# Optimization experiments

Measured on AMD Instinct MI355X. Metric: run time of the kernel, lower is better.

The kernel has to match this reference:

```python
import jax, jax.numpy as jnp
import numpy as np

EPS = 1e-12  # torch F.normalize eps

def _cam(fmap, w):
    # torch: sum over C of w[1,C,R,1,1] * fmap[B,C,1,H,W] -> (B,R,H,W)
    # expressed as an efficient contraction (1x1 conv / GEMM)
    return jnp.einsum('bchw,rc->brhw', fmap, w)

def _embedding(fmap, w, b):
    pooled = fmap.mean(axis=(-2, -1))           # (B,C) AdaptiveAvgPool2d(1)
    return pooled @ w.T + b                      # (B,R)

def _certainty(cam):
    B, R = cam.shape[:2]
    flat = cam.reshape(B, R, -1)
    return jnp.std(flat, axis=-1, ddof=1)        # torch .std() is unbiased

def _avgpool_to(x, out_hw):
    # adaptive avg pool with integer ratio == reshape-mean
    B, R, H, W = x.shape
    oh, ow = out_hw
    return x.reshape(B, R, oh, H // oh, ow, W // ow).mean(axis=(3, 5))

def _link(low_cam, high_cam):
    low_cam = jax.lax.stop_gradient(low_cam)
    high_cam = jax.lax.stop_gradient(high_cam)
    if low_cam.shape[2:] != high_cam.shape[2:]:
        low_cam = _avgpool_to(low_cam, high_cam.shape[2:])
    B = low_cam.shape[0]
    lo = low_cam.reshape(B, low_cam.shape[1], -1)
    hi = high_cam.reshape(B, high_cam.shape[1], -1)
    lo = lo / jnp.maximum(jnp.linalg.norm(lo, axis=-1, keepdims=True), EPS)
    hi = hi / jnp.maximum(jnp.linalg.norm(hi, axis=-1, keepdims=True), EPS)
    return jnp.einsum('bmi,bni->mn', lo, hi) / B

def setup_inputs() -> dict:
    key = jax.random.key(0)
    ks = jax.random.split(key, 6)
    B, R = 64, 128
    chans = [512, 1024, 2048]
    hws = [28, 14, 7]
    inp = {}
    for l in range(3):
        inp[f'fmap{l}'] = jax.random.normal(ks[l], (B, chans[l], hws[l], hws[l]), dtype=jnp.float32)
        inp[f'w{l}'] = jax.random.normal(ks[3 + l], (R, chans[l]), dtype=jnp.float32) * 0.02
        inp[f'b{l}'] = jnp.zeros((R,), dtype=jnp.float32)
    return inp

def reference(fmap0, fmap1, fmap2, w0, b0, w1, b1, w2, b2):
    fmaps = [fmap0, fmap1, fmap2]
    ws = [w0, w1, w2]
    bs = [b0, b1, b2]
    embeddings = [_embedding(f, w, b) for f, w, b in zip(fmaps, ws, bs)]
    cams = [_cam(f, w) for f, w in zip(fmaps, ws)]
    certainties = [_certainty(c) for c in cams]
    links = [_link(cams[l - 1], cams[l]) for l in range(1, 3)]
    return (*embeddings, *certainties, *links)
```

## Files before the change

kernel.cpp:

```cpp
#include <hip/hip_runtime.h>
#include <stdint.h>

#define R 128
#define NB 64

#define CAM0_OFF 0
#define CAM1_OFF 6422528
#define CAM2_OFF 8028160
#define POOL0_OFF 8429568
#define POOL1_OFF 10035200
#define WB_OFF    10436608
#define PART_OFF  10665984
#define NORM_OFF  12763136

typedef __bf16 bf16;
typedef bf16 v2bf __attribute__((ext_vector_type(2)));
typedef bf16 v8bf __attribute__((ext_vector_type(8)));
typedef float f4v __attribute__((ext_vector_type(4)));

#define ASM_BARRIER() asm volatile("s_waitcnt lgkmcnt(0)\n\ts_barrier" ::: "memory")

__global__ void prep_w(const float* __restrict__ w0, const float* __restrict__ w1,
                       const float* __restrict__ w2, bf16* __restrict__ wb) {
    int id = blockIdx.x * 256 + threadIdx.x;
    float v;
    if (id < 65536)       v = w0[id];
    else if (id < 196608) v = w1[id - 65536];
    else                  v = w2[id - 196608];
    wb[id] = (bf16)v;
}

__global__ __launch_bounds__(512) void cam_gemm(
    const float* __restrict__ f0, const float* __restrict__ f1,
    const float* __restrict__ f2, const bf16* __restrict__ wb,
    float* __restrict__ ws) {
    __shared__ bf16 ldsB[2][64 * 72];

    int bid = blockIdx.x, tid = threadIdx.x;
    int lvl, b, i0;
    if (bid < 64)       { lvl = 2; b = bid; i0 = 0; }
    else if (bid < 320) { int t = bid - 64; lvl = 1; b = t >> 2;
                          int ti = t & 3; i0 = ti < 3 ? ti * 64 : 132; }
    else                { int t = bid - 320; lvl = 0; b = t / 13;
                          int ti = t - b * 13; i0 = ti < 12 ? ti * 64 : 720; }
    const int C  = (lvl == 0) ? 512 : (lvl == 1) ? 1024 : 2048;
    const int HW = (lvl == 0) ? 784 : (lvl == 1) ? 196  : 49;
    const float* fmap = (lvl == 0) ? f0 : (lvl == 1) ? f1 : f2;
    const bf16*  wbl  = wb + ((lvl == 0) ? 0 : (lvl == 1) ? 65536 : 196608);
    float* cam = ws + ((lvl == 0) ? CAM0_OFF : (lvl == 1) ? CAM1_OFF : CAM2_OFF);

    int d = tid >> 4;
    int ku2 = d * 2;
    int i4 = (tid & 15) * 4;
    int gbase = b * C * HW + ku2 * HW + i0 + i4;
    int ldsd[4];
    int i4c[4];
#pragma unroll
    for (int e = 0; e < 4; ++e) {
        int i = i4 + e;
        int grp = (d >> 2) ^ ((i >> 3) & 7);
        ldsd[e] = i * 72 + grp * 8 + (d & 3) * 2;
        i4c[e] = min(i, 48);
    }
    const int lane = tid & 63, wave = tid >> 6;
    const int lm = lane & 15, q = lane >> 4;
    const int wm = (wave >> 1) * 32, wn = (wave & 1) * 32;
    int irow[2], ixor[2];
#pragma unroll
    for (int sn = 0; sn < 2; ++sn) {
        irow[sn] = wn + sn * 16 + lm;
        ixor[sn] = (irow[sn] >> 3) & 7;
    }
    const bf16* arow[2];
#pragma unroll
    for (int sm = 0; sm < 2; ++sm)
        arow[sm] = wbl + (wm + sm * 16 + lm) * C + q * 8;

    auto loadT = [&](int kc, float4 (&r)[2]) {
        if (HW != 49) {
            const float* p = fmap + gbase + kc * HW;
            r[0] = *(const float4*)p;
            r[1] = *(const float4*)(p + HW);
        } else {
            const float* p = fmap + b * C * 49 + (kc + ku2) * 49;
            r[0].x = p[i4c[0]]; r[0].y = p[i4c[1]];
            r[0].z = p[i4c[2]]; r[0].w = p[i4c[3]];
            r[1].x = p[49 + i4c[0]]; r[1].y = p[49 + i4c[1]];
            r[1].z = p[49 + i4c[2]]; r[1].w = p[49 + i4c[3]];
        }
    };
    auto stage = [&](float4 (&r)[2], bf16* buf) {
        v2bf t0 = { (bf16)r[0].x, (bf16)r[1].x };
        v2bf t1 = { (bf16)r[0].y, (bf16)r[1].y };
        v2bf t2 = { (bf16)r[0].z, (bf16)r[1].z };
        v2bf t3 = { (bf16)r[0].w, (bf16)r[1].w };
        *(v2bf*)&buf[ldsd[0]] = t0;
        *(v2bf*)&buf[ldsd[1]] = t1;
        *(v2bf*)&buf[ldsd[2]] = t2;
        *(v2bf*)&buf[ldsd[3]] = t3;
    };

    f4v acc[2][2] = {};
    auto comp = [&](int kc, const bf16* buf) {
#pragma unroll
        for (int ks = 0; ks < 64; ks += 32) {
            v8bf af[2];
#pragma unroll
            for (int sm = 0; sm < 2; ++sm)
                af[sm] = *(const v8bf*)(arow[sm] + kc + ks);
            v8bf bfr[2];
#pragma unroll
            for (int sn = 0; sn < 2; ++sn) {
                int grp = (q + ((ks >> 5) << 2)) ^ ixor[sn];
                bfr[sn] = *(const v8bf*)&buf[irow[sn] * 72 + grp * 8];
            }
#pragma unroll
            for (int sm = 0; sm < 2; ++sm)
#pragma unroll
                for (int sn = 0; sn < 2; ++sn)
                    acc[sm][sn] = __builtin_amdgcn_mfma_f32_16x16x32_bf16(
                        af[sm], bfr[sn], acc[sm][sn], 0, 0, 0);
        }
    };

    const int nIter = C >> 6;
    float4 rT[4][2];
    loadT(0, rT[0]); loadT(64, rT[1]); loadT(128, rT[2]); loadT(192, rT[3]);
    for (int t = 0; t < nIter; t += 4) {
#pragma unroll
        for (int u = 0; u < 4; ++u) {
            stage(rT[u], ldsB[u & 1]);
            ASM_BARRIER();
            if (t + u + 4 < nIter) loadT((t + u + 4) << 6, rT[u]);
            comp((t + u) << 6, ldsB[u & 1]);
        }
    }
#pragma unroll
    for (int sn = 0; sn < 2; ++sn) {
        int i_n = i0 + irow[sn];
        if (i_n < HW) {
            int base = (b * R) * HW + i_n;
#pragma unroll
            for (int sm = 0; sm < 2; ++sm) {
#pragma unroll
                for (int reg = 0; reg < 4; ++reg) {
                    int r = wm + sm * 16 + q * 4 + reg;
                    cam[base + r * HW] = acc[sm][sn][reg];
                }
            }
        }
    }
}

__global__ __launch_bounds__(256) void post_k(
    float* __restrict__ ws, const float* __restrict__ b0,
    const float* __restrict__ b1, const float* __restrict__ b2,
    float* __restrict__ out) {
    __shared__ float plds[4 * 784];
    int gw = blockIdx.x * 4 + (threadIdx.x >> 6);
    int lane = threadIdx.x & 63;
    float* myl = plds + (threadIdx.x >> 6) * 784;
    int lvl = gw >> 13, row = gw & 8191;
    const int HW = (lvl == 0) ? 784 : (lvl == 1) ? 196 : 49;
    const float* cam = ws + ((lvl == 0) ? CAM0_OFF : (lvl == 1) ? CAM1_OFF : CAM2_OFF)
                        + (long)row * HW;
    float s = 0.f, ss = 0.f;
    for (int j = lane; j < HW; j += 64) {
        float v = cam[j]; s += v; ss += v * v; myl[j] = v;
    }
#pragma unroll
    for (int o = 32; o; o >>= 1) { s += __shfl_xor(s, o); ss += __shfl_xor(ss, o); }
    if (lane == 0) {
        const float* bias = (lvl == 0) ? b0 : (lvl == 1) ? b1 : b2;
        float mean = s / (float)HW;
        out[lvl * 8192 + row] = mean + bias[row & 127];
        float var = fmaxf(ss - s * mean, 0.f) / (float)(HW - 1);
        out[24576 + lvl * 8192 + row] = sqrtf(var);
        if (lvl >= 1)
            ws[NORM_OFF + (lvl - 1) * 8192 + row] = 1.0f / fmaxf(sqrtf(ss), 1e-12f);
    }
    if (lvl <= 1) {
        const int OP = (lvl == 0) ? 196 : 49;
        const int OW = (lvl == 0) ? 14 : 7;
        const int IW = (lvl == 0) ? 28 : 14;
        float vals[4]; float ssp = 0.f; int cnt = 0;
        for (int p = lane; p < OP; p += 64) {
            int oh = p / OW, ow = p - oh * OW;
            int i0 = oh * 2 * IW + ow * 2;
            float v = (myl[i0] + myl[i0 + 1] + myl[i0 + IW] + myl[i0 + IW + 1]) * 0.25f;
            vals[cnt++] = v; ssp += v * v;
        }
#pragma unroll
        for (int o = 32; o; o >>= 1) ssp += __shfl_xor(ssp, o);
        float inv = 1.0f / fmaxf(sqrtf(ssp), 1e-12f);
        float* dst = ws + ((lvl == 0) ? POOL0_OFF : POOL1_OFF) + (long)row * OP;
        cnt = 0;
        for (int p = lane; p < OP; p += 64) dst[p] = vals[cnt++] * inv;
    }
}

__device__ inline v8bf load_frag8(const float* __restrict__ row, int k0, int K) {
    v8bf f;
    if (k0 + 8 <= K && (K & 3) == 0) {
        float4 a = *(const float4*)(row + k0);
        float4 c = *(const float4*)(row + k0 + 4);
        f[0] = (bf16)a.x; f[1] = (bf16)a.y; f[2] = (bf16)a.z; f[3] = (bf16)a.w;
        f[4] = (bf16)c.x; f[5] = (bf16)c.y; f[6] = (bf16)c.z; f[7] = (bf16)c.w;
    } else {
#pragma unroll
        for (int j = 0; j < 8; ++j)
            f[j] = (k0 + j < K) ? (bf16)row[k0 + j] : (bf16)0.f;
    }
    return f;
}

__global__ __launch_bounds__(256) void link_mfma_k(const float* __restrict__ ws,
                                                   float* __restrict__ part) {
    int bid = blockIdx.x, tid = threadIdx.x;
    int lk = bid >> 7, rem = bid & 127;
    int b = rem >> 1, mh = rem & 1;
    const int K = lk ? 49 : 196;
    const float* lo = ws + (lk ? POOL1_OFF : POOL0_OFF) + (long)(b * 128 + mh * 64) * K;
    const float* hi = ws + (lk ? CAM2_OFF : CAM1_OFF) + (long)b * 128 * K;
    const float* nrmp = ws + NORM_OFF + lk * 8192 + b * 128;
    int lane = tid & 63, wv = tid >> 6;
    int lm = lane & 15, q = lane >> 4;
    int wm = (wv >> 1) * 32, wn = (wv & 1) * 64;
    f4v acc[2][4] = {};
    for (int kc = 0; kc < K; kc += 32) {
        v8bf af[2], bff[4];
#pragma unroll
        for (int sm = 0; sm < 2; ++sm)
            af[sm] = load_frag8(lo + (long)(wm + sm * 16 + lm) * K, kc + q * 8, K);
#pragma unroll
        for (int sn = 0; sn < 4; ++sn)
            bff[sn] = load_frag8(hi + (long)(wn + sn * 16 + lm) * K, kc + q * 8, K);
#pragma unroll
        for (int sm = 0; sm < 2; ++sm)
#pragma unroll
            for (int sn = 0; sn < 4; ++sn)
                acc[sm][sn] = __builtin_amdgcn_mfma_f32_16x16x32_bf16(
                    af[sm], bff[sn], acc[sm][sn], 0, 0, 0);
    }
    float* pb = part + (long)b * 32768 + lk * 16384;
#pragma unroll
    for (int sn = 0; sn < 4; ++sn) {
        int n = wn + sn * 16 + lm;
        float sh = nrmp[n];
#pragma unroll
        for (int sm = 0; sm < 2; ++sm) {
#pragma unroll
            for (int reg = 0; reg < 4; ++reg) {
                int m = mh * 64 + wm + sm * 16 + q * 4 + reg;
                pb[m * 128 + n] = acc[sm][sn][reg] * sh;
            }
        }
    }
}

__global__ void linkred_k(const float* __restrict__ part, float* __restrict__ out) {
    int id = blockIdx.x * 256 + threadIdx.x;
    float s0 = 0.f, s1 = 0.f, s2 = 0.f, s3 = 0.f;
#pragma unroll
    for (int b = 0; b < 64; b += 4) {
        s0 += part[(long)(b + 0) * 32768 + id];
        s1 += part[(long)(b + 1) * 32768 + id];
        s2 += part[(long)(b + 2) * 32768 + id];
        s3 += part[(long)(b + 3) * 32768 + id];
    }
    out[49152 + id] = (s0 + s1 + s2 + s3) * (1.0f / 64.0f);
}

extern "C" void kernel_launch(void* const* d_in, const int* in_sizes, int n_in,
                              void* d_out, int out_size, void* d_ws, size_t ws_size,
                              hipStream_t stream) {
    const float* f0 = (const float*)d_in[0];
    const float* w0 = (const float*)d_in[1];
    const float* b0 = (const float*)d_in[2];
    const float* f1 = (const float*)d_in[3];
    const float* w1 = (const float*)d_in[4];
    const float* b1 = (const float*)d_in[5];
    const float* f2 = (const float*)d_in[6];
    const float* w2 = (const float*)d_in[7];
    const float* b2 = (const float*)d_in[8];
    float* ws = (float*)d_ws;
    float* out = (float*)d_out;
    bf16* wb = (bf16*)(ws + WB_OFF);

    prep_w<<<1792, 256, 0, stream>>>(w0, w1, w2, wb);
    cam_gemm<<<1152, 512, 0, stream>>>(f0, f1, f2, wb, ws);
    post_k<<<6144, 256, 0, stream>>>(ws, b0, b1, b2, out);
    link_mfma_k<<<256, 256, 0, stream>>>(ws, ws + PART_OFF);
    linkred_k<<<128, 256, 0, stream>>>(ws + PART_OFF, out);
}
```

Before: 296.6 us.

## Fuse CAM statistics and pooling into GEMM epilogue, atomically reduce link outputs

The GEMM now tiles spatial positions in 56-wide chunks aligned to image rows. Its epilogue computes per-row sums, sums of squares and 2x2 pooled values from an LDS tile, accumulating them with atomics. This stops the level-0 CAM from being written to global memory, and the separate post kernel becomes a small finalize kernel. The link kernel applies both normalisations and atomically adds into the output, which removes the partial buffer and its reduction kernel. The cost is atomic contention, extra work in the GEMM epilogue, and more GEMM blocks because of the 56-wide tiling.

```diff
diff --git a/kernel.cpp b/kernel.cpp
--- a/kernel.cpp
+++ b/kernel.cpp
@@ -4,14 +4,16 @@
 #define R 128
 #define NB 64
 
-#define CAM0_OFF 0
-#define CAM1_OFF 6422528
-#define CAM2_OFF 8028160
-#define POOL0_OFF 8429568
-#define POOL1_OFF 10035200
-#define WB_OFF    10436608
-#define PART_OFF  10665984
-#define NORM_OFF  12763136
+#define CAM1_OFF  0
+#define CAM2_OFF  1605632
+#define POOL0_OFF 2007040
+#define POOL1_OFF 3612672
+#define WB_OFF    4014080
+#define ACCS_OFF  4243456
+#define ACCQ_OFF  4268032
+#define PSQ_OFF   4292608
+#define INVHI_OFF 4308992
+#define INVLO_OFF 4325376
 
 typedef __bf16 bf16;
 typedef bf16 v2bf __attribute__((ext_vector_type(2)));
@@ -21,8 +23,11 @@
 #define ASM_BARRIER() asm volatile("s_waitcnt lgkmcnt(0)\n\ts_barrier" ::: "memory")
 
 __global__ void prep_w(const float* __restrict__ w0, const float* __restrict__ w1,
-                       const float* __restrict__ w2, bf16* __restrict__ wb) {
+                       const float* __restrict__ w2, bf16* __restrict__ wb,
+                       float* __restrict__ ws, float* __restrict__ out) {
     int id = blockIdx.x * 256 + threadIdx.x;
+    if (id < 65536) ws[ACCS_OFF + id] = 0.f;
+    if (id < 32768) out[49152 + id] = 0.f;
     float v;
     if (id < 65536)       v = w0[id];
     else if (id < 196608) v = w1[id - 65536];
@@ -34,25 +39,26 @@
     const float* __restrict__ f0, const float* __restrict__ f1,
     const float* __restrict__ f2, const bf16* __restrict__ wb,
     float* __restrict__ ws) {
-    __shared__ bf16 ldsB[2][64 * 72];
+    __shared__ __align__(16) char ldsRaw[34816];
+#define LBUF(u) ((bf16*)ldsRaw + (u) * (64 * 72))
 
     int bid = blockIdx.x, tid = threadIdx.x;
-    int lvl, b, i0;
-    if (bid < 64)       { lvl = 2; b = bid; i0 = 0; }
+    int lvl, b, i0, VW;
+    if (bid < 64)       { lvl = 2; b = bid; i0 = 0; VW = 49; }
     else if (bid < 320) { int t = bid - 64; lvl = 1; b = t >> 2;
-                          int ti = t & 3; i0 = ti < 3 ? ti * 64 : 132; }
-    else                { int t = bid - 320; lvl = 0; b = t / 13;
-                          int ti = t - b * 13; i0 = ti < 12 ? ti * 64 : 720; }
+                          int ti = t & 3; i0 = ti * 56; VW = ti < 3 ? 56 : 28; }
+    else                { int t = bid - 320; lvl = 0; b = t / 14;
+                          int ti = t - b * 14; i0 = ti * 56; VW = 56; }
     const int C  = (lvl == 0) ? 512 : (lvl == 1) ? 1024 : 2048;
     const int HW = (lvl == 0) ? 784 : (lvl == 1) ? 196  : 49;
     const float* fmap = (lvl == 0) ? f0 : (lvl == 1) ? f1 : f2;
     const bf16*  wbl  = wb + ((lvl == 0) ? 0 : (lvl == 1) ? 65536 : 196608);
-    float* cam = ws + ((lvl == 0) ? CAM0_OFF : (lvl == 1) ? CAM1_OFF : CAM2_OFF);
 
     int d = tid >> 4;
     int ku2 = d * 2;
     int i4 = (tid & 15) * 4;
-    int gbase = b * C * HW + ku2 * HW + i0 + i4;
+    int i4eff = min(i4, VW - 4);
+    int gbase = b * C * HW + ku2 * HW + i0 + i4eff;
     int ldsd[4];
     int i4c[4];
 #pragma unroll
@@ -77,7 +83,7 @@
         arow[sm] = wbl + (wm + sm * 16 + lm) * C + q * 8;
 
     auto loadT = [&](int kc, float4 (&r)[2]) {
-        if (HW != 49) {
+        if (lvl != 2) {
             const float* p = fmap + gbase + kc * HW;
             r[0] = *(const float4*)p;
             r[1] = *(const float4*)(p + HW);
@@ -129,74 +135,98 @@
     for (int t = 0; t < nIter; t += 4) {
 #pragma unroll
         for (int u = 0; u < 4; ++u) {
-            stage(rT[u], ldsB[u & 1]);
+            stage(rT[u], LBUF(u & 1));
             ASM_BARRIER();
             if (t + u + 4 < nIter) loadT((t + u + 4) << 6, rT[u]);
-            comp((t + u) << 6, ldsB[u & 1]);
-        }
-    }
-#pragma unroll
-    for (int sn = 0; sn < 2; ++sn) {
-        int i_n = i0 + irow[sn];
-        if (i_n < HW) {
-            int base = (b * R) * HW + i_n;
-#pragma unroll
-            for (int sm = 0; sm < 2; ++sm) {
-#pragma unroll
-                for (int reg = 0; reg < 4; ++reg) {
-                    int r = wm + sm * 16 + q * 4 + reg;
-                    cam[base + r * HW] = acc[sm][sn][reg];
-                }
+            comp((t + u) << 6, LBUF(u & 1));
+        }
+    }
+
+    __syncthreads();
+    float* tile = (float*)ldsRaw;
+#pragma unroll
+    for (int sn = 0; sn < 2; ++sn)
+#pragma unroll
+        for (int sm = 0; sm < 2; ++sm)
+#pragma unroll
+            for (int reg = 0; reg < 4; ++reg)
+                tile[(wm + sm * 16 + q * 4 + reg) * 68 + wn + sn * 16 + lm] =
+                    acc[sm][sn][reg];
+    __syncthreads();
+
+    int row = tid >> 2, seg = tid & 3;
+    long grow = (long)b * 128 + row;
+    const float* trow = tile + row * 68;
+    float* camrow = (lvl == 1) ? ws + CAM1_OFF + grow * 196 + i0
+                  : (lvl == 2) ? ws + CAM2_OFF + grow * 49 : (float*)0;
+    float s = 0.f, qq = 0.f;
+    const f4v* tr4 = (const f4v*)(trow + seg * 16);
+#pragma unroll
+    for (int g = 0; g < 4; ++g) {
+        f4v v4 = tr4[g];
+#pragma unroll
+        for (int e = 0; e < 4; ++e) {
+            int col = seg * 16 + g * 4 + e;
+            if (col < VW) {
+                float v = v4[e];
+                s += v; qq += v * v;
+                if (lvl) camrow[col] = v;
             }
         }
     }
-}
-
-__global__ __launch_bounds__(256) void post_k(
+    s += __shfl_xor(s, 1);  s += __shfl_xor(s, 2);
+    qq += __shfl_xor(qq, 1); qq += __shfl_xor(qq, 2);
+    if (seg == 0) {
+        atomicAdd(&ws[ACCS_OFF + lvl * 8192 + grow], s);
+        atomicAdd(&ws[ACCQ_OFF + lvl * 8192 + grow], qq);
+    }
+    if (lvl == 0) {
+        float ps = 0.f;
+        float* prow = ws + POOL0_OFF + grow * 196 + (i0 / 56) * 14;
+        for (int j = seg; j < 14; j += 4) {
+            float v = 0.25f * (trow[2 * j] + trow[2 * j + 1] +
+                               trow[28 + 2 * j] + trow[28 + 2 * j + 1]);
+            prow[j] = v; ps += v * v;
+        }
+        ps += __shfl_xor(ps, 1); ps += __shfl_xor(ps, 2);
+        if (seg == 0) atomicAdd(&ws[PSQ_OFF + grow], ps);
+    } else if (lvl == 1) {
+        float ps = 0.f;
+        int tt = i0 / 56;
+        int npj = (VW == 56) ? 14 : 7;
+        for (int pj = seg; pj < npj; pj += 4) {
+            int sub = pj / 7, jj = pj - sub * 7;
+            const float* tr2 = trow + sub * 28;
+            float v = 0.25f * (tr2[2 * jj] + tr2[2 * jj + 1] +
+                               tr2[14 + 2 * jj] + tr2[14 + 2 * jj + 1]);
+            ws[POOL1_OFF + grow * 49 + (2 * tt + sub) * 7 + jj] = v;
+            ps += v * v;
+        }
+        ps += __shfl_xor(ps, 1); ps += __shfl_xor(ps, 2);
+        if (seg == 0) atomicAdd(&ws[PSQ_OFF + 8192 + grow], ps);
+    }
+#undef LBUF
+}
+
+__global__ __launch_bounds__(256) void finalize_k(
     float* __restrict__ ws, const float* __restrict__ b0,
     const float* __restrict__ b1, const float* __restrict__ b2,
     float* __restrict__ out) {
-    __shared__ float plds[4 * 784];
-    int gw = blockIdx.x * 4 + (threadIdx.x >> 6);
-    int lane = threadIdx.x & 63;
-    float* myl = plds + (threadIdx.x >> 6) * 784;
-    int lvl = gw >> 13, row = gw & 8191;
-    const int HW = (lvl == 0) ? 784 : (lvl == 1) ? 196 : 49;
-    const float* cam = ws + ((lvl == 0) ? CAM0_OFF : (lvl == 1) ? CAM1_OFF : CAM2_OFF)
-                        + (long)row * HW;
-    float s = 0.f, ss = 0.f;
-    for (int j = lane; j < HW; j += 64) {
-        float v = cam[j]; s += v; ss += v * v; myl[j] = v;
-    }
-#pragma unroll
-    for (int o = 32; o; o >>= 1) { s += __shfl_xor(s, o); ss += __shfl_xor(ss, o); }
-    if (lane == 0) {
-        const float* bias = (lvl == 0) ? b0 : (lvl == 1) ? b1 : b2;
-        float mean = s / (float)HW;
-        out[lvl * 8192 + row] = mean + bias[row & 127];
-        float var = fmaxf(ss - s * mean, 0.f) / (float)(HW - 1);
-        out[24576 + lvl * 8192 + row] = sqrtf(var);
-        if (lvl >= 1)
-            ws[NORM_OFF + (lvl - 1) * 8192 + row] = 1.0f / fmaxf(sqrtf(ss), 1e-12f);
-    }
-    if (lvl <= 1) {
-        const int OP = (lvl == 0) ? 196 : 49;
-        const int OW = (lvl == 0) ? 14 : 7;
-        const int IW = (lvl == 0) ? 28 : 14;
-        float vals[4]; float ssp = 0.f; int cnt = 0;
-        for (int p = lane; p < OP; p += 64) {
-            int oh = p / OW, ow = p - oh * OW;
-            int i0 = oh * 2 * IW + ow * 2;
-            float v = (myl[i0] + myl[i0 + 1] + myl[i0 + IW] + myl[i0 + IW + 1]) * 0.25f;
-            vals[cnt++] = v; ssp += v * v;
-        }
-#pragma unroll
-        for (int o = 32; o; o >>= 1) ssp += __shfl_xor(ssp, o);
-        float inv = 1.0f / fmaxf(sqrtf(ssp), 1e-12f);
-        float* dst = ws + ((lvl == 0) ? POOL0_OFF : POOL1_OFF) + (long)row * OP;
-        cnt = 0;
-        for (int p = lane; p < OP; p += 64) dst[p] = vals[cnt++] * inv;
-    }
+    int id = blockIdx.x * 256 + threadIdx.x;
+    if (id < 16384) {
+        float qn = ws[PSQ_OFF + id];
+        ws[INVLO_OFF + id] = (1.0f / 64.0f) / fmaxf(sqrtf(qn), 1e-12f);
+    }
+    int lvl = id >> 13, row = id & 8191;
+    float HWf = (lvl == 0) ? 784.f : (lvl == 1) ? 196.f : 49.f;
+    float s = ws[ACCS_OFF + id], qq = ws[ACCQ_OFF + id];
+    float mean = s / HWf;
+    const float* bias = (lvl == 0) ? b0 : (lvl == 1) ? b1 : b2;
+    out[id] = mean + bias[row & 127];
+    float var = fmaxf(qq - s * mean, 0.f) / (HWf - 1.f);
+    out[24576 + id] = sqrtf(var);
+    if (lvl >= 1)
+        ws[INVHI_OFF + (lvl - 1) * 8192 + row] = 1.0f / fmaxf(sqrtf(qq), 1e-12f);
 }
 
 __device__ inline v8bf load_frag8(const float* __restrict__ row, int k0, int K) {
@@ -215,14 +245,15 @@
 }
 
 __global__ __launch_bounds__(256) void link_mfma_k(const float* __restrict__ ws,
-                                                   float* __restrict__ part) {
+                                                   float* __restrict__ out) {
     int bid = blockIdx.x, tid = threadIdx.x;
     int lk = bid >> 7, rem = bid & 127;
     int b = rem >> 1, mh = rem & 1;
     const int K = lk ? 49 : 196;
     const float* lo = ws + (lk ? POOL1_OFF : POOL0_OFF) + (long)(b * 128 + mh * 64) * K;
     const float* hi = ws + (lk ? CAM2_OFF : CAM1_OFF) + (long)b * 128 * K;
-    const float* nrmp = ws + NORM_OFF + lk * 8192 + b * 128;
+    const float* ihi = ws + INVHI_OFF + lk * 8192 + b * 128;
+    const float* ilo = ws + INVLO_OFF + lk * 8192 + b * 128 + mh * 64;
     int lane = tid & 63, wv = tid >> 6;
     int lm = lane & 15, q = lane >> 4;
     int wm = (wv >> 1) * 32, wn = (wv & 1) * 64;
@@ -242,33 +273,26 @@
                 acc[sm][sn] = __builtin_amdgcn_mfma_f32_16x16x32_bf16(
                     af[sm], bff[sn], acc[sm][sn], 0, 0, 0);
     }
-    float* pb = part + (long)b * 32768 + lk * 16384;
+    float fl[2][4];
+#pragma unroll
+    for (int sm = 0; sm < 2; ++sm)
+#pragma unroll
+        for (int reg = 0; reg < 4; ++reg)
+            fl[sm][reg] = ilo[wm + sm * 16 + q * 4 + reg];
+    float* ob = out + 49152 + lk * 16384;
 #pragma unroll
     for (int sn = 0; sn < 4; ++sn) {
         int n = wn + sn * 16 + lm;
-        float sh = nrmp[n];
+        float sh = ihi[n];
 #pragma unroll
         for (int sm = 0; sm < 2; ++sm) {
 #pragma unroll
             for (int reg = 0; reg < 4; ++reg) {
                 int m = mh * 64 + wm + sm * 16 + q * 4 + reg;
-                pb[m * 128 + n] = acc[sm][sn][reg] * sh;
+                atomicAdd(&ob[m * 128 + n], acc[sm][sn][reg] * sh * fl[sm][reg]);
             }
         }
     }
-}
-
-__global__ void linkred_k(const float* __restrict__ part, float* __restrict__ out) {
-    int id = blockIdx.x * 256 + threadIdx.x;
-    float s0 = 0.f, s1 = 0.f, s2 = 0.f, s3 = 0.f;
-#pragma unroll
-    for (int b = 0; b < 64; b += 4) {
-        s0 += part[(long)(b + 0) * 32768 + id];
-        s1 += part[(long)(b + 1) * 32768 + id];
-        s2 += part[(long)(b + 2) * 32768 + id];
-        s3 += part[(long)(b + 3) * 32768 + id];
-    }
-    out[49152 + id] = (s0 + s1 + s2 + s3) * (1.0f / 64.0f);
 }
 
 extern "C" void kernel_launch(void* const* d_in, const int* in_sizes, int n_in,
@@ -287,9 +311,8 @@
     float* out = (float*)d_out;
     bf16* wb = (bf16*)(ws + WB_OFF);
 
-    prep_w<<<1792, 256, 0, stream>>>(w0, w1, w2, wb);
-    cam_gemm<<<1152, 512, 0, stream>>>(f0, f1, f2, wb, ws);
-    post_k<<<6144, 256, 0, stream>>>(ws, b0, b1, b2, out);
-    link_mfma_k<<<256, 256, 0, stream>>>(ws, ws + PART_OFF);
-    linkred_k<<<128, 256, 0, stream>>>(ws + PART_OFF, out);
-}
+    prep_w<<<1792, 256, 0, stream>>>(w0, w1, w2, wb, ws, out);
+    cam_gemm<<<1216, 512, 0, stream>>>(f0, f1, f2, wb, ws);
+    finalize_k<<<96, 256, 0, stream>>>(ws, b0, b1, b2, out);
+    link_mfma_k<<<256, 256, 0, stream>>>(ws, out);
+}
```

Measured after the change: 285.6 us. 3.7% less time.
